# Performance work log

Measured on AMD Instinct MI355X. Metric: run time of the kernel, lower is better.

The kernel has to match this reference:

```python
import jax, jax.numpy as jnp
import numpy as np

N_SUP, N_SUB, LATENT, OUT = 256, 1024, 512, 200


def list_of_distances(X, Y):
    # squared Euclidean pairwise distances: (len(X), len(Y))
    xx = jnp.sum(X * X, axis=1, keepdims=True)          # (n, 1)
    yy = jnp.sum(Y * Y, axis=1)[None, :]                # (1, m)
    return xx - 2.0 * (X @ Y.T) + yy


def setup_inputs() -> dict:
    key = jax.random.key(0)
    ks = jax.random.split(key, 7)
    x = jax.random.normal(ks[0], (32768, LATENT), dtype=jnp.float32)
    sup_prototypes = jax.random.uniform(ks[1], (N_SUP, LATENT), dtype=jnp.float32)
    sub_prototypes = jax.random.uniform(ks[2], (N_SUB, LATENT), dtype=jnp.float32)
    lim1 = 1.0 / np.sqrt(N_SUP)
    lim2 = 1.0 / np.sqrt(N_SUB)
    W1 = jax.random.uniform(ks[3], (OUT, N_SUP), dtype=jnp.float32, minval=-lim1, maxval=lim1)
    b1 = jax.random.uniform(ks[4], (OUT,), dtype=jnp.float32, minval=-lim1, maxval=lim1)
    W2 = jax.random.uniform(ks[5], (OUT, N_SUB), dtype=jnp.float32, minval=-lim2, maxval=lim2)
    b2 = jax.random.uniform(ks[6], (OUT,), dtype=jnp.float32, minval=-lim2, maxval=lim2)
    return {"x": x, "sup_prototypes": sup_prototypes, "sub_prototypes": sub_prototypes,
            "W1": W1, "b1": b1, "W2": W2, "b2": b2}


def reference(x, sup_prototypes, sub_prototypes, W1, b1, W2, b2):
    sup_input_dist = list_of_distances(x, sup_prototypes)   # (B, n_sup)
    sub_input_dist = list_of_distances(x, sub_prototypes)   # (B, n_sub)
    sup_out = sup_input_dist @ W1.T + b1                     # (B, out)
    sub_out = sub_input_dist @ W2.T + b2                     # (B, out)
    sub_clones = jax.lax.stop_gradient(sub_prototypes)
    super_sub_dist = list_of_distances(sup_prototypes, sub_clones)  # (n_sup, n_sub)
    r1 = jnp.mean(jnp.min(sub_input_dist, axis=0))
    r2 = jnp.mean(jnp.min(sub_input_dist, axis=1))
    r3 = jnp.mean(jnp.min(super_sub_dist, axis=1))
    r4 = jnp.mean(jnp.min(super_sub_dist, axis=0))
    return (sub_out, sup_out, r1, r2, r3, r4)
```

## Files before the change

kernel.cpp:

```cpp
#include <hip/hip_runtime.h>
#include <stdint.h>

#define BATCH   32768
#define NSUP    256
#define NSUB    1024
#define LATENT  512
#define NOUT    200
#define SUP_OFF ((size_t)BATCH * NOUT)

typedef unsigned short u16;
typedef __attribute__((ext_vector_type(8))) __bf16 bf16x8;
typedef __attribute__((ext_vector_type(4))) float  floatx4;

typedef const __attribute__((address_space(1))) void* gptr_t;
typedef __attribute__((address_space(3))) void* sptr_t;

__device__ __forceinline__ void gload16(const void* g, void* l) {
  __builtin_amdgcn_global_load_lds((gptr_t)g, (sptr_t)l, 16, 0, 0);
}

__device__ __forceinline__ floatx4 mfma_bf16(bf16x8 a, bf16x8 b, floatx4 c) {
  return __builtin_amdgcn_mfma_f32_16x16x32_bf16(a, b, c, 0, 0, 0);
}

__device__ __forceinline__ u16 f2bf(float f) {
  unsigned int u = __float_as_uint(f);
  u += 0x7FFFu + ((u >> 16) & 1u);
  return (u16)(u >> 16);
}

__device__ __forceinline__ size_t bfoff(int c, int k) {
  return (size_t)(c >> 4) * 8192 + (size_t)((k >> 5) * 512)
       + (size_t)((((k >> 3) & 3) * 16 + (c & 15)) * 8) + (size_t)(k & 7);
}

__global__ __launch_bounds__(256) void k_setup(const float* __restrict__ sup,
    const float* __restrict__ sub, const float* __restrict__ W1,
    const float* __restrict__ W2, u16* __restrict__ sups, u16* __restrict__ subs,
    u16* __restrict__ Bf, float* __restrict__ MtF, float* __restrict__ xxsup,
    float* __restrict__ yys, unsigned int* __restrict__ minbuf,
    float* __restrict__ out4) {
  __shared__ float lw[8 * 128];
  int bx = blockIdx.x;
  if (bx >= 458) {
    int idx = bx - 458;
    if (idx >= 800) {
      int z = idx - 800;
      int k = (z & 1) * 256 + threadIdx.x;
      int o0 = 400 + (z >> 1) * 8;
      for (int oo = 0; oo < 8; oo++) Bf[bfoff(o0 + oo, k)] = 0;
      return;
    }
    int jc = idx & 7;
    int kb = (idx >> 3) & 1;
    int o0 = (idx >> 4) * 8;
    int k  = kb * 256 + threadIdx.x;
    const float* P; const float* W; int n, ow, nqs;
    if (o0 < 200) { P = sup; W = W1; n = NSUP;  ow = o0;       nqs = 5; }
    else          { P = sub; W = W2; n = NSUB;  ow = o0 - 200; nqs = 7; }
    int nq = 1 << nqs;
    int j0 = jc * nq;
    for (int i = threadIdx.x; i < 8 * nq; i += 256) {
      int oo = i >> nqs, j = i & (nq - 1);
      lw[oo * 128 + j] = W[(size_t)(ow + oo) * n + j0 + j];
    }
    __syncthreads();
    float a[8] = {};
    for (int j = 0; j < nq; j += 8) {
      float pv[8];
#pragma unroll
      for (int u = 0; u < 8; u++) pv[u] = P[(size_t)(j0 + j + u) * LATENT + k];
#pragma unroll
      for (int oo = 0; oo < 8; oo++) {
        float acc = 0.f;
#pragma unroll
        for (int u = 0; u < 8; u++) acc += pv[u] * lw[oo * 128 + j + u];
        a[oo] += acc;
      }
    }
#pragma unroll
    for (int oo = 0; oo < 8; oo++)
      MtF[((size_t)jc * 400 + o0 + oo) * 512 + k] = a[oo];
    return;
  }
  if (bx >= 320) {
    if (bx == 457) { if (threadIdx.x < 4) out4[threadIdx.x] = 0.f; return; }
    int i = (bx - 320) * 256 + threadIdx.x;
    if (i < BATCH + NSUP + 2 * NSUB) minbuf[i] = 0x7F800000u;
    return;
  }
  int row  = bx * 4 + (threadIdx.x >> 6);
  int lane = threadIdx.x & 63;
  const float* src; u16* dst; float* nrm; int subrow = -1;
  if (row < NSUP) { src = sup + (size_t)row * LATENT; dst = sups + (size_t)row * LATENT; nrm = xxsup + row; }
  else { int r = row - NSUP; subrow = r; src = sub + (size_t)r * LATENT; dst = subs + (size_t)r * LATENT; nrm = yys + r; }
  const float* s = src + lane * 8;
  float4 v0 = ((const float4*)s)[0];
  float4 v1 = ((const float4*)s)[1];
  float ss = v0.x*v0.x + v0.y*v0.y + v0.z*v0.z + v0.w*v0.w
           + v1.x*v1.x + v1.y*v1.y + v1.z*v1.z + v1.w*v1.w;
  uint4 o;
  o.x = (unsigned)f2bf(v0.x) | ((unsigned)f2bf(v0.y) << 16);
  o.y = (unsigned)f2bf(v0.z) | ((unsigned)f2bf(v0.w) << 16);
  o.z = (unsigned)f2bf(v1.x) | ((unsigned)f2bf(v1.y) << 16);
  o.w = (unsigned)f2bf(v1.z) | ((unsigned)f2bf(v1.w) << 16);
  *((uint4*)(dst + lane * 8)) = o;
  if (subrow >= 0) {
    size_t off = (size_t)(32 + (subrow >> 4)) * 8192 + (size_t)((lane >> 2) * 512)
               + (size_t)((((lane & 3) * 16) + (subrow & 15)) * 8);
    *((uint4*)(Bf + off)) = o;
  }
  for (int off = 32; off; off >>= 1) ss += __shfl_down(ss, off);
  if (lane == 0) *nrm = ss;
}

__global__ __launch_bounds__(256) void k_scc(const float* __restrict__ W1,
    const float* __restrict__ b1, const float* __restrict__ W2,
    const float* __restrict__ b2, const float* __restrict__ xxsup,
    const float* __restrict__ yys, float* __restrict__ sc, float* __restrict__ cc,
    const u16* __restrict__ sups, const u16* __restrict__ subs,
    const float* __restrict__ MtF, u16* __restrict__ Bf,
    unsigned int* __restrict__ rowmin, unsigned int* __restrict__ colsup) {
  __shared__ __align__(16) u16 lA[64 * 64];
  __shared__ __align__(16) u16 lB[128 * 64];
  int bx = blockIdx.x;
  if (bx >= 132) {
    int o = bx - 132;
    for (int k = threadIdx.x; k < 512; k += 256) {
      float s = 0.f;
#pragma unroll
      for (int c = 0; c < 8; c++) s += MtF[((size_t)c * 400 + o) * 512 + k];
      Bf[bfoff(o, k)] = f2bf(-2.f * s);
    }
    return;
  }
  if (bx >= 100) {
    int bid = bx - 100;
    int cb = bid & 7;
    size_t arow0 = (size_t)(bid >> 3) * 64;
    const u16* B = subs + (size_t)cb * 128 * LATENT;
    floatx4 acc[2][4] = {};
    int t = threadIdx.x, wave = t >> 6, lane = t & 63;
    int l16 = lane & 15, qq = lane >> 4;
    int wm = (wave >> 1) * 32, wn = (wave & 1) * 64;
    int sq = (lane & 7) ^ (lane >> 3);
    const u16* Ab = sups + arow0 * LATENT;
    int soffA[2], soffB[4]; u16 *dA[2], *dB[4];
#pragma unroll
    for (int i = 0; i < 2; i++) {
      int s = i * 256 + t;
      soffA[i] = (s >> 3) * LATENT + sq * 8;
      dA[i] = lA + (i * 256 + wave * 64) * 8;
    }
#pragma unroll
    for (int i = 0; i < 4; i++) {
      int s = i * 256 + t;
      soffB[i] = (s >> 3) * LATENT + sq * 8;
      dB[i] = lB + (i * 256 + wave * 64) * 8;
    }
    for (int k0 = 0; k0 < LATENT; k0 += 64) {
#pragma unroll
      for (int i = 0; i < 2; i++) gload16(Ab + soffA[i] + k0, dA[i]);
#pragma unroll
      for (int i = 0; i < 4; i++) gload16(B  + soffB[i] + k0, dB[i]);
      __syncthreads();
#pragma unroll
      for (int ks = 0; ks < 2; ks++) {
        bf16x8 af[2], bvv[4];
        int sw = ((ks * 4 + qq) ^ (l16 & 7)) * 8;
#pragma unroll
        for (int f = 0; f < 2; f++)
          af[f]  = *(const bf16x8*)(lA + (wm + f * 16 + l16) * 64 + sw);
#pragma unroll
        for (int f = 0; f < 4; f++)
          bvv[f] = *(const bf16x8*)(lB + (wn + f * 16 + l16) * 64 + sw);
#pragma unroll
        for (int fm = 0; fm < 2; fm++)
#pragma unroll
          for (int fn = 0; fn < 4; fn++)
            acc[fm][fn] = mfma_bf16(af[fm], bvv[fn], acc[fm][fn]);
      }
      __syncthreads();
    }
    int colb = cb * 128 + wn + l16;
    float yv[4];
#pragma unroll
    for (int fn = 0; fn < 4; fn++) yv[fn] = yys[colb + fn * 16];
    float cmin[4] = {3.4e38f, 3.4e38f, 3.4e38f, 3.4e38f};
#pragma unroll
    for (int fm = 0; fm < 2; fm++) {
#pragma unroll
      for (int r = 0; r < 4; r++) {
        int row = (int)arow0 + wm + fm * 16 + qq * 4 + r;
        float xvv = xxsup[row];
        float rmin = 3.4e38f;
#pragma unroll
        for (int fn = 0; fn < 4; fn++) {
          float d = xvv - 2.0f * acc[fm][fn][r] + yv[fn];
          rmin = fminf(rmin, d);
          cmin[fn] = fminf(cmin[fn], d);
        }
        for (int off = 1; off < 16; off <<= 1) rmin = fminf(rmin, __shfl_xor(rmin, off));
        if (l16 == 0) atomicMin(rowmin + BATCH + row, __float_as_uint(rmin));
      }
    }
#pragma unroll
    for (int fn = 0; fn < 4; fn++) {
      float v = cmin[fn];
      v = fminf(v, __shfl_xor(v, 16));
      v = fminf(v, __shfl_xor(v, 32));
      if (qq == 0) atomicMin(colsup + colb + fn * 16, __float_as_uint(v));
    }
    return;
  }
  int wave = threadIdx.x >> 6, lane = threadIdx.x & 63;
  int o = bx * 4 + wave;
  if (o >= 400) return;
  int n; const float* Wr; const float* yy;
  if (o < 200) { n = NSUP; Wr = W1 + (size_t)o * NSUP; yy = xxsup; }
  else         { n = NSUB; Wr = W2 + (size_t)(o - 200) * NSUB; yy = yys; }
  float s = 0.f, c = 0.f;
  for (int j = lane; j < n; j += 64) { float w = Wr[j]; s += w; c += w * yy[j]; }
  for (int off = 32; off; off >>= 1) { s += __shfl_down(s, off); c += __shfl_down(c, off); }
  if (lane == 0) { sc[o] = s; cc[o] = c + ((o < 200) ? b1[o] : b2[o - 200]); }
}

__global__ __launch_bounds__(512, 2) void k_gemm_x(const float* __restrict__ x,
    const u16* __restrict__ Bf, const float* __restrict__ yys,
    const float* __restrict__ sc, const float* __restrict__ cc,
    float* __restrict__ out, unsigned int* __restrict__ rowmin,
    unsigned int* __restrict__ colx) {
  __shared__ __align__(16) u16 lA[128 * 512];
  __shared__ float lxx[128];
  int t = threadIdx.x, wave = t >> 6, lane = t & 63;
  int l16 = lane & 15, qq = lane >> 4;
  int wr = wave >> 2, wc = wave & 3;
  size_t arow0 = (size_t)blockIdx.x * 128;

  const float* Ab = x + arow0 * LATENT;
#pragma unroll
  for (int i = 0; i < 16; i++) {
    int row = i * 8 + wave;
    const float* s = Ab + (size_t)row * LATENT + lane * 8;
    float4 v0 = ((const float4*)s)[0];
    float4 v1 = ((const float4*)s)[1];
    float ss = v0.x*v0.x + v0.y*v0.y + v0.z*v0.z + v0.w*v0.w
             + v1.x*v1.x + v1.y*v1.y + v1.z*v1.z + v1.w*v1.w;
    uint4 o;
    o.x = (unsigned)f2bf(v0.x) | ((unsigned)f2bf(v0.y) << 16);
    o.y = (unsigned)f2bf(v0.z) | ((unsigned)f2bf(v0.w) << 16);
    o.z = (unsigned)f2bf(v1.x) | ((unsigned)f2bf(v1.y) << 16);
    o.w = (unsigned)f2bf(v1.z) | ((unsigned)f2bf(v1.w) << 16);
    *((uint4*)(lA + ((row * 64) + (lane ^ (row & 7))) * 8)) = o;
    for (int off = 32; off; off >>= 1) ss += __shfl_down(ss, off);
    if (lane == 0) lxx[row] = ss;
  }
  __syncthreads();

  float xv[4][4];
#pragma unroll
  for (int mf = 0; mf < 4; mf++)
#pragma unroll
    for (int r = 0; r < 4; r++) xv[mf][r] = lxx[wr * 64 + mf * 16 + qq * 4 + r];
  float rmreg[4][4];
#pragma unroll
  for (int mf = 0; mf < 4; mf++)
#pragma unroll
    for (int r = 0; r < 4; r++) rmreg[mf][r] = 3.4e38f;

#pragma unroll 1
  for (int p = 0; p < 6; p++) {
    floatx4 acc[4][4] = {};
    const u16* Bw = Bf + (size_t)(p * 16 + wc * 4) * 8192 + lane * 8;
#pragma unroll 2
    for (int k0 = 0; k0 < LATENT; k0 += 64) {
      bf16x8 bv[4][2];
#pragma unroll
      for (int nf = 0; nf < 4; nf++)
#pragma unroll
        for (int ks = 0; ks < 2; ks++)
          bv[nf][ks] = *(const bf16x8*)(Bw + nf * 8192 + k0 * 16 + ks * 512);
#pragma unroll
      for (int ks = 0; ks < 2; ks++) {
        bf16x8 a[4];
#pragma unroll
        for (int mf = 0; mf < 4; mf++) {
          int row = wr * 64 + mf * 16 + l16;
          int kc = (k0 >> 3) + ks * 4 + qq;
          a[mf] = *(const bf16x8*)(lA + ((row * 64) + (kc ^ (row & 7))) * 8);
        }
#pragma unroll
        for (int mf = 0; mf < 4; mf++)
#pragma unroll
          for (int nf = 0; nf < 4; nf++)
            acc[mf][nf] = mfma_bf16(a[mf], bv[nf][ks], acc[mf][nf]);
      }
    }
    if (p < 2) {
      int colbase = p * 256 + wc * 64;
#pragma unroll
      for (int nf = 0; nf < 4; nf++) {
        int c = colbase + nf * 16 + l16;
        if (c < 400) {
          float scv = sc[c], ccv = cc[c];
#pragma unroll
          for (int mf = 0; mf < 4; mf++)
#pragma unroll
            for (int r = 0; r < 4; r++) {
              size_t row = arow0 + wr * 64 + mf * 16 + qq * 4 + r;
              float v = acc[mf][nf][r] + xv[mf][r] * scv + ccv;
              size_t idx = (c < 200) ? (SUP_OFF + row * NOUT + c)
                                     : (row * NOUT + (c - 200));
              out[idx] = v;
            }
        }
      }
    } else {
      int colbase = p * 256 + wc * 64 - 512;
#pragma unroll
      for (int nf = 0; nf < 4; nf++) {
        int cs = colbase + nf * 16 + l16;
        float yv = yys[cs];
        float cmin = 3.4e38f;
#pragma unroll
        for (int mf = 0; mf < 4; mf++)
#pragma unroll
          for (int r = 0; r < 4; r++) {
            float d = xv[mf][r] - 2.0f * acc[mf][nf][r] + yv;
            rmreg[mf][r] = fminf(rmreg[mf][r], d);
            cmin = fminf(cmin, d);
          }
        cmin = fminf(cmin, __shfl_xor(cmin, 16));
        cmin = fminf(cmin, __shfl_xor(cmin, 32));
        if (qq == 0) atomicMin(colx + cs, __float_as_uint(cmin));
      }
    }
  }
#pragma unroll
  for (int mf = 0; mf < 4; mf++)
#pragma unroll
    for (int r = 0; r < 4; r++) {
      float v = rmreg[mf][r];
      v = fminf(v, __shfl_xor(v, 1));
      v = fminf(v, __shfl_xor(v, 2));
      v = fminf(v, __shfl_xor(v, 4));
      v = fminf(v, __shfl_xor(v, 8));
      if (l16 == 0)
        atomicMin(rowmin + arow0 + wr * 64 + mf * 16 + qq * 4 + r, __float_as_uint(v));
    }
}

__global__ __launch_bounds__(256) void k_final2(const unsigned int* __restrict__ rowmin,
    const unsigned int* __restrict__ colx, const unsigned int* __restrict__ colsup,
    float* __restrict__ out4) {
  int bx = blockIdx.x, t = threadIdx.x;
  const unsigned int* src; int n; float scale; int slot;
  if (bx < 32)      { src = rowmin + bx * 1024; n = 1024; scale = 1.f / BATCH; slot = 1; }
  else if (bx == 32){ src = colx;               n = 1024; scale = 1.f / NSUB;  slot = 0; }
  else if (bx == 33){ src = rowmin + BATCH;     n = 256;  scale = 1.f / NSUP;  slot = 2; }
  else              { src = colsup;             n = 1024; scale = 1.f / NSUB;  slot = 3; }
  float s = 0.f;
  for (int i = t; i < n; i += 256) s += __uint_as_float(src[i]);
  __shared__ float red[4];
  for (int off = 32; off; off >>= 1) s += __shfl_down(s, off);
  if ((t & 63) == 0) red[t >> 6] = s;
  __syncthreads();
  if (t == 0) atomicAdd(out4 + slot, (red[0] + red[1] + red[2] + red[3]) * scale);
}

extern "C" void kernel_launch(void* const* d_in, const int* in_sizes, int n_in,
                              void* d_out, int out_size, void* d_ws, size_t ws_size,
                              hipStream_t stream) {
  const float* x   = (const float*)d_in[0];
  const float* sup = (const float*)d_in[1];
  const float* sub = (const float*)d_in[2];
  const float* W1  = (const float*)d_in[3];
  const float* b1  = (const float*)d_in[4];
  const float* W2  = (const float*)d_in[5];
  const float* b2  = (const float*)d_in[6];
  float* out = (float*)d_out;

  char* p = (char*)d_ws;
  u16* Bf    = (u16*)p;            p += (size_t)(512 + NSUB) * LATENT * 2;
  u16* subs  = (u16*)p;            p += (size_t)NSUB * LATENT * 2;
  u16* sups  = (u16*)p;            p += (size_t)NSUP * LATENT * 2;
  float* xxsup = (float*)p;        p += NSUP * 4;
  float* yys   = (float*)p;        p += NSUB * 4;
  float* sc    = (float*)p;        p += 512 * 4;
  float* cc    = (float*)p;        p += 512 * 4;
  unsigned int* rowmin = (unsigned int*)p; p += (size_t)(BATCH + NSUP) * 4;
  unsigned int* colx   = (unsigned int*)p; p += (size_t)NSUB * 4;
  unsigned int* colsup = (unsigned int*)p; p += (size_t)NSUB * 4;
  float* MtF   = (float*)p;        p += (size_t)8 * 400 * 512 * 4;

  float* out4 = out + 2 * SUP_OFF;

  hipLaunchKernelGGL(k_setup, dim3(1286), dim3(256), 0, stream,
                     sup, sub, W1, W2, sups, subs, Bf, MtF, xxsup, yys, rowmin, out4);
  hipLaunchKernelGGL(k_scc, dim3(532), dim3(256), 0, stream,
                     W1, b1, W2, b2, xxsup, yys, sc, cc, sups, subs, MtF, Bf,
                     rowmin, colsup);
  hipLaunchKernelGGL(k_gemm_x, dim3(BATCH / 128), dim3(512), 0, stream,
                     x, Bf, yys, sc, cc, out, rowmin, colx);
  hipLaunchKernelGGL(k_final2, dim3(35), dim3(256), 0, stream, rowmin, colx, colsup, out4);
}
```

Before: 107.2 us.

## Retile x GEMM to 64-row blocks with all eight waves spanning columns

The main GEMM kernel now processes 64 rows of x per block instead of 128. All 8 waves split the column dimension (512 columns per pass, 3 passes instead of 6), which halves LDS use per block to allow more resident blocks and doubles the grid. The row-min atomics now fire once per sub-prototype pass instead of once at the end, and the xx values are reloaded from LDS each pass to cut live registers. In exchange, each B tile is reused across half as many rows, so B traffic from L2 roughly doubles, and there are more row-min atomics.

```diff
diff --git a/kernel.cpp b/kernel.cpp
--- a/kernel.cpp
+++ b/kernel.cpp
@@ -230,16 +230,16 @@
     const float* __restrict__ sc, const float* __restrict__ cc,
     float* __restrict__ out, unsigned int* __restrict__ rowmin,
     unsigned int* __restrict__ colx) {
-  __shared__ __align__(16) u16 lA[128 * 512];
-  __shared__ float lxx[128];
+  __shared__ __align__(16) u16 lA[64 * 512];
+  __shared__ float lxx[64];
   int t = threadIdx.x, wave = t >> 6, lane = t & 63;
   int l16 = lane & 15, qq = lane >> 4;
-  int wr = wave >> 2, wc = wave & 3;
-  size_t arow0 = (size_t)blockIdx.x * 128;
+  int wc = wave;
+  size_t arow0 = (size_t)blockIdx.x * 64;
 
   const float* Ab = x + arow0 * LATENT;
 #pragma unroll
-  for (int i = 0; i < 16; i++) {
+  for (int i = 0; i < 8; i++) {
     int row = i * 8 + wave;
     const float* s = Ab + (size_t)row * LATENT + lane * 8;
     float4 v0 = ((const float4*)s)[0];
@@ -257,21 +257,10 @@
   }
   __syncthreads();
 
-  float xv[4][4];
-#pragma unroll
-  for (int mf = 0; mf < 4; mf++)
-#pragma unroll
-    for (int r = 0; r < 4; r++) xv[mf][r] = lxx[wr * 64 + mf * 16 + qq * 4 + r];
-  float rmreg[4][4];
-#pragma unroll
-  for (int mf = 0; mf < 4; mf++)
-#pragma unroll
-    for (int r = 0; r < 4; r++) rmreg[mf][r] = 3.4e38f;
-
 #pragma unroll 1
-  for (int p = 0; p < 6; p++) {
+  for (int p = 0; p < 3; p++) {
     floatx4 acc[4][4] = {};
-    const u16* Bw = Bf + (size_t)(p * 16 + wc * 4) * 8192 + lane * 8;
+    const u16* Bw = Bf + (size_t)(p * 32 + wc * 4) * 8192 + lane * 8;
 #pragma unroll 2
     for (int k0 = 0; k0 < LATENT; k0 += 64) {
       bf16x8 bv[4][2];
@@ -285,7 +274,7 @@
         bf16x8 a[4];
 #pragma unroll
         for (int mf = 0; mf < 4; mf++) {
-          int row = wr * 64 + mf * 16 + l16;
+          int row = mf * 16 + l16;
           int kc = (k0 >> 3) + ks * 4 + qq;
           a[mf] = *(const bf16x8*)(lA + ((row * 64) + (kc ^ (row & 7))) * 8);
         }
@@ -296,8 +285,13 @@
             acc[mf][nf] = mfma_bf16(a[mf], bv[nf][ks], acc[mf][nf]);
       }
     }
-    if (p < 2) {
-      int colbase = p * 256 + wc * 64;
+    float xr[4][4];
+#pragma unroll
+    for (int mf = 0; mf < 4; mf++)
+#pragma unroll
+      for (int r = 0; r < 4; r++) xr[mf][r] = lxx[mf * 16 + qq * 4 + r];
+    if (p == 0) {
+      int colbase = wc * 64;
 #pragma unroll
       for (int nf = 0; nf < 4; nf++) {
         int c = colbase + nf * 16 + l16;
@@ -307,8 +301,8 @@
           for (int mf = 0; mf < 4; mf++)
 #pragma unroll
             for (int r = 0; r < 4; r++) {
-              size_t row = arow0 + wr * 64 + mf * 16 + qq * 4 + r;
-              float v = acc[mf][nf][r] + xv[mf][r] * scv + ccv;
+              size_t row = arow0 + mf * 16 + qq * 4 + r;
+              float v = acc[mf][nf][r] + xr[mf][r] * scv + ccv;
               size_t idx = (c < 200) ? (SUP_OFF + row * NOUT + c)
                                      : (row * NOUT + (c - 200));
               out[idx] = v;
@@ -316,7 +310,12 @@
         }
       }
     } else {
-      int colbase = p * 256 + wc * 64 - 512;
+      int colbase = (p - 1) * 512 + wc * 64;
+      float rm[4][4];
+#pragma unroll
+      for (int mf = 0; mf < 4; mf++)
+#pragma unroll
+        for (int r = 0; r < 4; r++) rm[mf][r] = 3.4e38f;
 #pragma unroll
       for (int nf = 0; nf < 4; nf++) {
         int cs = colbase + nf * 16 + l16;
@@ -326,28 +325,28 @@
         for (int mf = 0; mf < 4; mf++)
 #pragma unroll
           for (int r = 0; r < 4; r++) {
-            float d = xv[mf][r] - 2.0f * acc[mf][nf][r] + yv;
-            rmreg[mf][r] = fminf(rmreg[mf][r], d);
+            float d = xr[mf][r] - 2.0f * acc[mf][nf][r] + yv;
+            rm[mf][r] = fminf(rm[mf][r], d);
             cmin = fminf(cmin, d);
           }
         cmin = fminf(cmin, __shfl_xor(cmin, 16));
         cmin = fminf(cmin, __shfl_xor(cmin, 32));
         if (qq == 0) atomicMin(colx + cs, __float_as_uint(cmin));
       }
-    }
-  }
-#pragma unroll
-  for (int mf = 0; mf < 4; mf++)
-#pragma unroll
-    for (int r = 0; r < 4; r++) {
-      float v = rmreg[mf][r];
-      v = fminf(v, __shfl_xor(v, 1));
-      v = fminf(v, __shfl_xor(v, 2));
-      v = fminf(v, __shfl_xor(v, 4));
-      v = fminf(v, __shfl_xor(v, 8));
-      if (l16 == 0)
-        atomicMin(rowmin + arow0 + wr * 64 + mf * 16 + qq * 4 + r, __float_as_uint(v));
-    }
+#pragma unroll
+      for (int mf = 0; mf < 4; mf++)
+#pragma unroll
+        for (int r = 0; r < 4; r++) {
+          float v = rm[mf][r];
+          v = fminf(v, __shfl_xor(v, 1));
+          v = fminf(v, __shfl_xor(v, 2));
+          v = fminf(v, __shfl_xor(v, 4));
+          v = fminf(v, __shfl_xor(v, 8));
+          if (l16 == 0)
+            atomicMin(rowmin + arow0 + mf * 16 + qq * 4 + r, __float_as_uint(v));
+        }
+    }
+  }
 }
 
 __global__ __launch_bounds__(256) void k_final2(const unsigned int* __restrict__ rowmin,
@@ -400,7 +399,7 @@
   hipLaunchKernelGGL(k_scc, dim3(532), dim3(256), 0, stream,
                      W1, b1, W2, b2, xxsup, yys, sc, cc, sups, subs, MtF, Bf,
                      rowmin, colsup);
-  hipLaunchKernelGGL(k_gemm_x, dim3(BATCH / 128), dim3(512), 0, stream,
+  hipLaunchKernelGGL(k_gemm_x, dim3(BATCH / 64), dim3(512), 0, stream,
                      x, Bf, yys, sc, cc, out, rowmin, colx);
   hipLaunchKernelGGL(k_final2, dim3(35), dim3(256), 0, stream, rowmin, colx, colsup, out4);
 }
```

New measurement: 149.4 us. 39.3% more time.
